# Optimization experiments

Measured on AMD Instinct MI355X. Metric: run time of the kernel, lower is better.

Reference implementation:

```python
import jax, jax.numpy as jnp
import numpy as np

D_MODEL = 1024
NUM_HEADS = 16
HEAD_DIM = D_MODEL // NUM_HEADS
FF_DIM = 4096
EPS = 1e-5


def _layer_norm(x, gamma, beta):
    mu = jnp.mean(x, axis=-1, keepdims=True)
    var = jnp.var(x, axis=-1, keepdims=True)
    return (x - mu) * jax.lax.rsqrt(var + EPS) * gamma + beta


def setup_inputs() -> dict:
    key0 = jax.random.key(0)
    ks = jax.random.split(key0, 20)
    s = 0.02
    B, S = 2, 2048
    inp = {
        'value': jax.random.normal(ks[0], (B, S, D_MODEL), jnp.float32),
        'key': jax.random.normal(ks[1], (B, S, D_MODEL), jnp.float32),
        'query': jax.random.normal(ks[2], (B, S, D_MODEL), jnp.float32),
        # attention projections (stored [in, out]; y = x @ W + b)
        'wq': jax.random.normal(ks[3], (D_MODEL, D_MODEL), jnp.float32) * s,
        'bq': jnp.zeros((D_MODEL,), jnp.float32),
        'wk': jax.random.normal(ks[4], (D_MODEL, D_MODEL), jnp.float32) * s,
        'bk': jnp.zeros((D_MODEL,), jnp.float32),
        'wv': jax.random.normal(ks[5], (D_MODEL, D_MODEL), jnp.float32) * s,
        'bv': jnp.zeros((D_MODEL,), jnp.float32),
        'wo': jax.random.normal(ks[6], (D_MODEL, D_MODEL), jnp.float32) * s,
        'bo': jnp.zeros((D_MODEL,), jnp.float32),
        # layernorm 1
        'g1': jnp.ones((D_MODEL,), jnp.float32),
        'beta1': jnp.zeros((D_MODEL,), jnp.float32),
        # feed-forward
        'w1': jax.random.normal(ks[7], (D_MODEL, FF_DIM), jnp.float32) * s,
        'b1': jnp.zeros((FF_DIM,), jnp.float32),
        'w2': jax.random.normal(ks[8], (FF_DIM, D_MODEL), jnp.float32) * s,
        'b2': jnp.zeros((D_MODEL,), jnp.float32),
        # layernorm 2
        'g2': jnp.ones((D_MODEL,), jnp.float32),
        'beta2': jnp.zeros((D_MODEL,), jnp.float32),
    }
    return inp


def reference(value, key, query, wq, bq, wk, bk, wv, bv, wo, bo,
              g1, beta1, w1, b1, w2, b2, g2, beta2):
    B, S, _ = query.shape
    # QKV projections -> [B, S, H, Dh]
    Q = (query @ wq + bq).reshape(B, S, NUM_HEADS, HEAD_DIM)
    K = (key @ wk + bk).reshape(B, S, NUM_HEADS, HEAD_DIM)
    V = (value @ wv + bv).reshape(B, S, NUM_HEADS, HEAD_DIM)
    # scaled dot-product attention (full score matrix, as in source)
    energy = jnp.einsum('bqhd,bkhd->bhqk', Q, K) / jnp.sqrt(jnp.float32(HEAD_DIM))
    attn = jax.nn.softmax(energy, axis=-1)
    out = jnp.einsum('bhqk,bkhd->bqhd', attn, V).reshape(B, S, D_MODEL)
    attn_out = out @ wo + bo
    # residual + norm1 (dropout is identity in eval)
    x = _layer_norm(attn_out + query, g1, beta1)
    # feed-forward
    ff = jax.nn.relu(x @ w1 + b1) @ w2 + b2
    # residual + norm2
    return _layer_norm(ff + x, g2, beta2)
```

## Files before the change

kernel.cpp:

```cpp
#include <hip/hip_runtime.h>
#include <hip/hip_bf16.h>
#include <cstdint>
#include <math.h>

typedef __bf16 bf16_t;
typedef __attribute__((ext_vector_type(2))) __bf16 bf16x2;
typedef __attribute__((ext_vector_type(4))) __bf16 bf16x4;
typedef __attribute__((ext_vector_type(8))) __bf16 bf16x8;
typedef __attribute__((ext_vector_type(4))) float f32x4;
typedef __attribute__((ext_vector_type(16))) float f32x16;
typedef __attribute__((ext_vector_type(2))) int int2v;
typedef __attribute__((ext_vector_type(4))) int int4v;

#define B_SZ 2
#define S_SZ 2048
#define D_MODEL 1024
#define NUM_HEADS 16
#define HEAD_DIM 64
#define FF_DIM 4096
#define M_ROWS (B_SZ * S_SZ)

#define CF 0.180336880f
#define THRC 2.0f

__device__ __forceinline__ float fexp2(float x) { return __builtin_amdgcn_exp2f(x); }

__device__ __forceinline__ void gload_lds16(const void* g, void* lds) {
    __builtin_amdgcn_global_load_lds(
        (const __attribute__((address_space(1))) void*)(uintptr_t)g,
        (__attribute__((address_space(3))) void*)(uint32_t)(uintptr_t)lds,
        16, 0, 0);
}

__device__ __forceinline__ f32x4 mfma16(bf16x8 a, bf16x8 b, f32x4 c) {
    return __builtin_amdgcn_mfma_f32_16x16x32_bf16(a, b, c, 0, 0, 0);
}
__device__ __forceinline__ f32x16 mfma32(bf16x8 a, bf16x8 b, f32x16 c) {
    return __builtin_amdgcn_mfma_f32_32x32x16_bf16(a, b, c, 0, 0, 0);
}
__device__ __forceinline__ int2v plswap(int a, int b) {
    return __builtin_amdgcn_permlane32_swap(a, b, false, false);
}
__device__ __forceinline__ int packbf(float a, float b) {
    bf16x2 t; t[0] = (bf16_t)a; t[1] = (bf16_t)b;
    return __builtin_bit_cast(int, t);
}

__device__ __forceinline__ int xcd_swz(int lin, int nwg) {
    return (lin & 7) * (nwg >> 3) + (lin >> 3);
}

__global__ __launch_bounds__(256) void cast3_f32_bf16(const float* __restrict__ in0,
                                                      const float* __restrict__ in1,
                                                      const float* __restrict__ in2,
                                                      bf16_t* __restrict__ out0,
                                                      bf16_t* __restrict__ out1,
                                                      bf16_t* __restrict__ out2) {
    int which = blockIdx.x >> 12;
    int blk = blockIdx.x & 4095;
    const float* in = which == 0 ? in0 : which == 1 ? in1 : in2;
    bf16_t* out = which == 0 ? out0 : which == 1 ? out1 : out2;
    size_t i = ((size_t)blk * 256 + threadIdx.x) * 4;
    float4 v = *(const float4*)(in + i);
    bf16x4 o;
    o[0] = (bf16_t)v.x; o[1] = (bf16_t)v.y; o[2] = (bf16_t)v.z; o[3] = (bf16_t)v.w;
    *(bf16x4*)(out + i) = o;
}

__global__ __launch_bounds__(256) void transpose_cast_w4(const float* __restrict__ W0,
                                                         const float* __restrict__ W1,
                                                         const float* __restrict__ W2,
                                                         const float* __restrict__ W3,
                                                         bf16_t* __restrict__ T0,
                                                         bf16_t* __restrict__ T1,
                                                         bf16_t* __restrict__ T2,
                                                         bf16_t* __restrict__ T3) {
    __shared__ float t[32][33];
    const int K = 1024, N = 1024;
    const float* W = blockIdx.z == 0 ? W0 : blockIdx.z == 1 ? W1 : blockIdx.z == 2 ? W2 : W3;
    bf16_t* WT = blockIdx.z == 0 ? T0 : blockIdx.z == 1 ? T1 : blockIdx.z == 2 ? T2 : T3;
    int tid = threadIdx.x;
    int rr = tid >> 3, cc = (tid & 7) * 4;
    int k0 = blockIdx.x * 32, n0 = blockIdx.y * 32;
    float4 v = *(const float4*)(W + (size_t)(k0 + rr) * N + n0 + cc);
    t[rr][cc + 0] = v.x; t[rr][cc + 1] = v.y; t[rr][cc + 2] = v.z; t[rr][cc + 3] = v.w;
    __syncthreads();
    bf16x4 o;
    o[0] = (bf16_t)t[cc + 0][rr]; o[1] = (bf16_t)t[cc + 1][rr];
    o[2] = (bf16_t)t[cc + 2][rr]; o[3] = (bf16_t)t[cc + 3][rr];
    *(bf16x4*)(WT + (size_t)(n0 + rr) * K + k0 + cc) = o;
}

__global__ __launch_bounds__(256) void transpose_cast_w(const float* __restrict__ W,
                                                        bf16_t* __restrict__ WT,
                                                        int K, int N) {
    __shared__ float t[32][33];
    int tid = threadIdx.x;
    int rr = tid >> 3, cc = (tid & 7) * 4;
    int k0 = blockIdx.x * 32, n0 = blockIdx.y * 32;
    float4 v = *(const float4*)(W + (size_t)(k0 + rr) * N + n0 + cc);
    t[rr][cc + 0] = v.x; t[rr][cc + 1] = v.y; t[rr][cc + 2] = v.z; t[rr][cc + 3] = v.w;
    __syncthreads();
    bf16x4 o;
    o[0] = (bf16_t)t[cc + 0][rr]; o[1] = (bf16_t)t[cc + 1][rr];
    o[2] = (bf16_t)t[cc + 2][rr]; o[3] = (bf16_t)t[cc + 3][rr];
    *(bf16x4*)(WT + (size_t)(n0 + rr) * K + k0 + cc) = o;
}

__global__ __launch_bounds__(256) void transpose_v(const bf16_t* __restrict__ Vp,
                                                   bf16_t* __restrict__ VT) {
    __shared__ bf16_t t[32][34];
    int tid = threadIdx.x;
    int rr = tid >> 3, cc = (tid & 7) * 4;
    int bh = blockIdx.z;
    int b = bh >> 4, h = bh & 15;
    int s0 = blockIdx.x * 32, d0 = blockIdx.y * 32;
    bf16x4 v = *(const bf16x4*)(Vp + ((size_t)(b * S_SZ + s0 + rr)) * D_MODEL + h * HEAD_DIM + d0 + cc);
    t[rr][cc + 0] = v[0]; t[rr][cc + 1] = v[1]; t[rr][cc + 2] = v[2]; t[rr][cc + 3] = v[3];
    __syncthreads();
    bf16x4 o;
    o[0] = t[cc + 0][rr]; o[1] = t[cc + 1][rr]; o[2] = t[cc + 2][rr]; o[3] = t[cc + 3][rr];
    *(bf16x4*)(VT + ((size_t)(bh * HEAD_DIM + d0 + rr)) * S_SZ + s0 + cc) = o;
}

template<int BNF, bool RELU, bool OUT_BF16, bool OUT_F32>
__device__ __forceinline__ void gemm_core256(const bf16_t* __restrict__ A, int lda,
                                             const bf16_t* __restrict__ Bt, int ldb,
                                             const float* __restrict__ bias, bool useBias,
                                             float* __restrict__ Cf,
                                             bf16_t* __restrict__ Cb,
                                             int N, int Klen, int m0, int n0,
                                             bf16_t* sA, bf16_t* sB) {
    const int tid = threadIdx.x;
    const int lane = tid & 63, w = tid >> 6;
    const int g = lane >> 4, r = lane & 15;
    const int wm = (w >> 2) * 128;
    const int wn = (w & 3) * (16 * BNF);
    const int ABUF = 8192;
    const int BBUF = (BNF == 4) ? 8192 : 4096;

    const bf16_t* Ablk = A + (size_t)m0 * lda;
    const bf16_t* Bblk = Bt + (size_t)n0 * ldb;
    const bf16_t* a0 = Ablk + (size_t)(tid >> 2) * lda + (tid & 3) * 8;
    const bf16_t* a1 = a0 + (size_t)128 * lda;
    const bf16_t* b0 = Bblk + (size_t)(tid >> 2) * ldb + (tid & 3) * 8;
    const bf16_t* b1 = b0 + (size_t)128 * ldb;

    f32x4 acc[8][BNF];
#pragma unroll
    for (int i = 0; i < 8; i++)
#pragma unroll
        for (int j = 0; j < BNF; j++)
#pragma unroll
            for (int e = 0; e < 4; e++) acc[i][j][e] = 0.f;

    auto stage = [&](int buf, int k0) {
        gload_lds16(a0 + k0, sA + buf * ABUF + tid * 8);
        gload_lds16(a1 + k0, sA + buf * ABUF + 4096 + tid * 8);
        gload_lds16(b0 + k0, sB + buf * BBUF + tid * 8);
        if (BNF == 4) gload_lds16(b1 + k0, sB + buf * BBUF + 4096 + tid * 8);
    };
    auto compute = [&](int buf) {
        bf16x8 a[8], b[BNF];
#pragma unroll
        for (int i = 0; i < 8; i++)
            a[i] = *(const bf16x8*)(sA + buf * ABUF + (wm + i * 16 + r) * 32 + g * 8);
#pragma unroll
        for (int j = 0; j < BNF; j++)
            b[j] = *(const bf16x8*)(sB + buf * BBUF + (wn + j * 16 + r) * 32 + g * 8);
#pragma unroll
        for (int i = 0; i < 8; i++)
#pragma unroll
            for (int j = 0; j < BNF; j++)
                acc[i][j] = mfma16(a[i], b[j], acc[i][j]);
    };

    const int nk = Klen >> 5;
    stage(0, 0);
    stage(1, 32);
    int bc = 0, bs = 2;
    for (int s = 0; s < nk; ++s) {
        if (s + 2 < nk) {
            stage(bs, (s + 2) * 32);
            if (BNF == 4) asm volatile("s_waitcnt vmcnt(8)" ::: "memory");
            else          asm volatile("s_waitcnt vmcnt(6)" ::: "memory");
        } else if (s + 1 < nk) {
            if (BNF == 4) asm volatile("s_waitcnt vmcnt(4)" ::: "memory");
            else          asm volatile("s_waitcnt vmcnt(3)" ::: "memory");
        } else {
            asm volatile("s_waitcnt vmcnt(0)" ::: "memory");
        }
        __builtin_amdgcn_s_barrier();
        __builtin_amdgcn_sched_barrier(0);
        compute(bc);
        __builtin_amdgcn_sched_barrier(0);
        __builtin_amdgcn_s_barrier();
        bc = (bc + 1 == 3) ? 0 : bc + 1;
        bs = (bs + 1 == 3) ? 0 : bs + 1;
    }

#pragma unroll
    for (int j = 0; j < BNF; j++) {
        int n = n0 + wn + j * 16 + r;
        float bv = useBias ? bias[n] : 0.f;
#pragma unroll
        for (int i = 0; i < 8; i++) {
#pragma unroll
            for (int rr = 0; rr < 4; rr++) {
                int mrow = m0 + wm + i * 16 + g * 4 + rr;
                float val = acc[i][j][rr] + bv;
                if (RELU) val = fmaxf(val, 0.f);
                if (OUT_F32) Cf[(size_t)mrow * N + n] = val;
                if (OUT_BF16) Cb[(size_t)mrow * N + n] = (bf16_t)val;
            }
        }
    }
}

template<int BNF, bool RELU, bool OUT_BF16, bool OUT_F32>
__global__ __launch_bounds__(512, 2) void gemm_bt256(const bf16_t* __restrict__ A, int lda,
                                                     const bf16_t* __restrict__ Bt, int ldb,
                                                     const float* __restrict__ bias,
                                                     float* __restrict__ Cf0,
                                                     float* __restrict__ Cf1,
                                                     bf16_t* __restrict__ Cb,
                                                     int N, int Klen) {
    __shared__ bf16_t sA[3 * 8192];
    __shared__ bf16_t sB[3 * ((BNF == 4) ? 8192 : 4096)];
    const int lin = blockIdx.x + gridDim.x * (blockIdx.y + gridDim.y * blockIdx.z);
    const int nwg = gridDim.x * gridDim.y * gridDim.z;
    const int swz = xcd_swz(lin, nwg);
    const int bx = swz % gridDim.x;
    const int rest = swz / gridDim.x;
    const int by = rest % gridDim.y;
    const int bz = rest / gridDim.y;
    const int koff = bz * Klen;
    gemm_core256<BNF, RELU, OUT_BF16, OUT_F32>(A + koff, lda, Bt + koff, ldb, bias, bz == 0,
                                               bz ? Cf1 : Cf0, Cb, N, Klen,
                                               bx * 256, by * (64 * BNF), sA, sB);
}

__global__ __launch_bounds__(512, 2) void gemm_qkv256(const bf16_t* __restrict__ A0,
                                                      const bf16_t* __restrict__ A1,
                                                      const bf16_t* __restrict__ A2,
                                                      const bf16_t* __restrict__ B0,
                                                      const bf16_t* __restrict__ B1,
                                                      const bf16_t* __restrict__ B2,
                                                      const float* __restrict__ b0,
                                                      const float* __restrict__ b1,
                                                      const float* __restrict__ b2,
                                                      bf16_t* __restrict__ C0,
                                                      bf16_t* __restrict__ C1,
                                                      bf16_t* __restrict__ C2) {
    __shared__ bf16_t sA[3 * 8192];
    __shared__ bf16_t sB[3 * 8192];
    const int lin = blockIdx.x + gridDim.x * (blockIdx.y + gridDim.y * blockIdx.z);
    const int nwg = gridDim.x * gridDim.y * gridDim.z;
    const int swz = xcd_swz(lin, nwg);
    const int bx = swz % gridDim.x;
    const int rest = swz / gridDim.x;
    const int by = rest % gridDim.y;
    const int bz = rest / gridDim.y;
    const bf16_t* A = bz == 0 ? A0 : bz == 1 ? A1 : A2;
    const bf16_t* Bt = bz == 0 ? B0 : bz == 1 ? B1 : B2;
    const float* bias = bz == 0 ? b0 : bz == 1 ? b1 : b2;
    bf16_t* C = bz == 0 ? C0 : bz == 1 ? C1 : C2;
    gemm_core256<4, false, true, false>(A, 1024, Bt, 1024, bias, true,
                                        nullptr, C, 1024, 1024, bx * 256, by * 256, sA, sB);
}

__device__ __forceinline__ void flash_tile(
    const char* kt, const char* vt, int l31, int hi,
    const bf16x8 (&bq)[4],
    f32x16& o0, f32x16& o1, float& mC, float& l_run)
{
    bf16x8 ak[4];
#pragma unroll
    for (int kb = 0; kb < 4; kb++)
        ak[kb] = *(const bf16x8*)(kt + l31 * 128 + (((kb << 1) | hi) ^ (l31 & 7)) * 16);
    bf16x8 av[4];
#pragma unroll
    for (int db = 0; db < 2; db++)
#pragma unroll
        for (int kb = 0; kb < 2; kb++)
            av[db * 2 + kb] = *(const bf16x8*)(vt + (db * 32 + l31) * 64 + ((((kb << 1) | hi)) ^ ((l31 >> 1) & 3)) * 16);

    f32x16 s;
#pragma unroll
    for (int e = 0; e < 16; e++) s[e] = 0.f;
#pragma unroll
    for (int kb = 0; kb < 4; kb++) s = mfma32(ak[kb], bq[kb], s);

    float ma = fmaxf(fmaxf(s[0], s[1]), fmaxf(s[2], s[3]));
    float mb = fmaxf(fmaxf(s[4], s[5]), fmaxf(s[6], s[7]));
    float mc = fmaxf(fmaxf(s[8], s[9]), fmaxf(s[10], s[11]));
    float md = fmaxf(fmaxf(s[12], s[13]), fmaxf(s[14], s[15]));
    float pmaxC = fmaxf(fmaxf(ma, mb), fmaxf(mc, md)) * CF;

    if (!__all(pmaxC <= mC + THRC)) {
        int2v pr = plswap(__float_as_int(pmaxC), __float_as_int(pmaxC));
        float rowmaxC = fmaxf(__int_as_float(pr[0]), __int_as_float(pr[1]));
        float mnewC = fmaxf(mC, rowmaxC);
        float alpha = fexp2(mC - mnewC);
        mC = mnewC;
        l_run *= alpha;
#pragma unroll
        for (int e = 0; e < 16; e++) { o0[e] *= alpha; o1[e] *= alpha; }
    }

#pragma unroll
    for (int e = 0; e < 16; e++) s[e] = fexp2(__builtin_fmaf(s[e], CF, -mC));
    float t0 = (s[0] + s[1]) + (s[2] + s[3]);
    float t1 = (s[4] + s[5]) + (s[6] + s[7]);
    float t2 = (s[8] + s[9]) + (s[10] + s[11]);
    float t3 = (s[12] + s[13]) + (s[14] + s[15]);
    l_run += (t0 + t1) + (t2 + t3);

#pragma unroll
    for (int kb2 = 0; kb2 < 2; kb2++) {
        const int bse = kb2 * 8;
        int W0 = packbf(s[bse + 0], s[bse + 1]);
        int W1 = packbf(s[bse + 2], s[bse + 3]);
        int W2 = packbf(s[bse + 4], s[bse + 5]);
        int W3 = packbf(s[bse + 6], s[bse + 7]);
        int2v r02 = plswap(W0, W2);
        int2v r13 = plswap(W1, W3);
        int4v fw; fw[0] = r02[0]; fw[1] = r13[0]; fw[2] = r02[1]; fw[3] = r13[1];
        bf16x8 pf = __builtin_bit_cast(bf16x8, fw);
        o0 = mfma32(av[kb2], pf, o0);
        o1 = mfma32(av[2 + kb2], pf, o1);
    }
}

__global__ __launch_bounds__(256) void flash_attn(const bf16_t* __restrict__ Qp,
                                                  const bf16_t* __restrict__ Kp,
                                                  const bf16_t* __restrict__ VT,
                                                  bf16_t* __restrict__ Oa) {
    __shared__ alignas(16) char lds[2][2][8192];
    const int tid = threadIdx.x;
    const int lane = tid & 63;
    const int wave = tid >> 6;
    const int half = wave >> 1;
    const int qt = wave & 1;
    const int l31 = lane & 31, hi = lane >> 5;

    const int lin = blockIdx.x + (blockIdx.y << 5) + (blockIdx.z << 9);
    const int swz = (lin & 7) * 128 + (lin >> 3);
    const int qb = swz & 31;
    const int h = (swz >> 5) & 15;
    const int b = swz >> 9;

    const int q0 = qb * 64 + qt * 32;

    const bf16_t* Qb = Qp + (size_t)b * S_SZ * D_MODEL + h * HEAD_DIM;
    const bf16_t* Kb = Kp + (size_t)b * S_SZ * D_MODEL + h * HEAD_DIM;
    const bf16_t* Vb = VT + ((size_t)(b * NUM_HEADS + h) * HEAD_DIM) * S_SZ;

    const int sh = wave & 1;
    const int skvbase = sh * (S_SZ / 2);
    const bool kRole = wave < 2;

    const bf16_t* src_run;
    size_t inner_stride;
    size_t tile_stride;
    char* dst0;
    char* dst1;
    if (kRole) {
        src_run = Kb + (size_t)(skvbase + (lane >> 3)) * D_MODEL + ((lane & 7) ^ (lane >> 3)) * 8;
        inner_stride = (size_t)8 * D_MODEL;
        tile_stride = (size_t)32 * D_MODEL;
        dst0 = &lds[0][sh][0] + lane * 16;
        dst1 = &lds[1][sh][0] + lane * 16;
    } else {
        src_run = Vb + (size_t)(lane >> 2) * S_SZ + skvbase + ((lane & 3) ^ ((lane >> 3) & 3)) * 8;
        inner_stride = (size_t)16 * S_SZ;
        tile_stride = 32;
        dst0 = &lds[0][sh][4096] + lane * 16;
        dst1 = &lds[1][sh][4096] + lane * 16;
    }

    bf16x8 bq[4];
#pragma unroll
    for (int kb = 0; kb < 4; kb++)
        bq[kb] = *(const bf16x8*)(Qb + (size_t)(q0 + l31) * D_MODEL + kb * 16 + hi * 8);

    f32x16 o0, o1;
#pragma unroll
    for (int e = 0; e < 16; e++) { o0[e] = 0.f; o1[e] = 0.f; }
    float mC = -1e30f, l_run = 0.f;

    const char* kt0 = &lds[0][half][0];
    const char* vt0 = &lds[0][half][4096];
    const char* kt1 = &lds[1][half][0];
    const char* vt1 = &lds[1][half][4096];

#pragma unroll
    for (int ii = 0; ii < 4; ii++)
        gload_lds16(src_run + ii * inner_stride, dst0 + ii * 1024);
    src_run += tile_stride;
    __syncthreads();

    for (int t = 0; t < 32; t += 2) {
#pragma unroll
        for (int ii = 0; ii < 4; ii++)
            gload_lds16(src_run + ii * inner_stride, dst1 + ii * 1024);
        src_run += tile_stride;
        flash_tile(kt0, vt0, l31, hi, bq, o0, o1, mC, l_run);
        __syncthreads();

        if (t + 2 < 32) {
#pragma unroll
            for (int ii = 0; ii < 4; ii++)
                gload_lds16(src_run + ii * inner_stride, dst0 + ii * 1024);
            src_run += tile_stride;
        }
        flash_tile(kt1, vt1, l31, hi, bq, o0, o1, mC, l_run);
        __syncthreads();
    }

    int2v lp = plswap(__float_as_int(l_run), __float_as_int(l_run));
    l_run = __int_as_float(lp[0]) + __int_as_float(lp[1]);

    float (*obuf)[2][64] = (float (*)[2][64])(&lds[0][0][0]);
    float (*mrg)[64][2] = (float (*)[64][2])(&lds[0][0][0] + 16384);
    if (half == 1) {
        mrg[qt][lane][0] = mC;
        mrg[qt][lane][1] = l_run;
#pragma unroll
        for (int e = 0; e < 16; e++) {
            obuf[e][qt][lane] = o0[e];
            obuf[16 + e][qt][lane] = o1[e];
        }
    }
    __syncthreads();
    if (half == 0) {
        const float m2C = mrg[qt][lane][0], l2 = mrg[qt][lane][1];
        const float mm = fmaxf(mC, m2C);
        const float e1 = fexp2(mC - mm);
        const float e2 = fexp2(m2C - mm);
        const float linv = 1.f / (l_run * e1 + l2 * e2);
        bf16_t* Orow = Oa + ((size_t)b * S_SZ + q0 + l31) * D_MODEL + h * HEAD_DIM;
#pragma unroll
        for (int db = 0; db < 2; db++) {
#pragma unroll
            for (int rq = 0; rq < 4; rq++) {
                bf16x4 st;
#pragma unroll
                for (int i = 0; i < 4; i++) {
                    const int e = rq * 4 + i;
                    const float own = db ? o1[e] : o0[e];
                    const float oth = obuf[db * 16 + e][qt][lane];
                    st[i] = (bf16_t)((own * e1 + oth * e2) * linv);
                }
                *(bf16x4*)(Orow + db * 32 + rq * 8 + hi * 4) = st;
            }
        }
    }
}

__global__ __launch_bounds__(256) void ln_fused(const float* __restrict__ A,
                                                const float* __restrict__ A2,
                                                const float* __restrict__ R,
                                                const float* __restrict__ gamma,
                                                const float* __restrict__ beta,
                                                float* __restrict__ Xf,
                                                bf16_t* __restrict__ Xb) {
    __shared__ float red[8];
    int row = blockIdx.x, tid = threadIdx.x;
    size_t base = (size_t)row * D_MODEL + tid * 4;
    float4 a = *(const float4*)(A + base);
    float4 rv = *(const float4*)(R + base);
    float v0 = a.x + rv.x, v1 = a.y + rv.y, v2 = a.z + rv.z, v3 = a.w + rv.w;
    if (A2) {
        float4 a2 = *(const float4*)(A2 + base);
        v0 += a2.x; v1 += a2.y; v2 += a2.z; v3 += a2.w;
    }
    float s = v0 + v1 + v2 + v3;
    float q = v0 * v0 + v1 * v1 + v2 * v2 + v3 * v3;
#pragma unroll
    for (int off = 32; off; off >>= 1) { s += __shfl_down(s, off); q += __shfl_down(q, off); }
    if ((tid & 63) == 0) { red[tid >> 6] = s; red[4 + (tid >> 6)] = q; }
    __syncthreads();
    s = red[0] + red[1] + red[2] + red[3];
    q = red[4] + red[5] + red[6] + red[7];
    float mean = s * (1.f / D_MODEL);
    float var = q * (1.f / D_MODEL) - mean * mean;
    float rstd = rsqrtf(var + 1e-5f);
    float4 gm = *(const float4*)(gamma + tid * 4);
    float4 bt = *(const float4*)(beta + tid * 4);
    float y0 = (v0 - mean) * rstd * gm.x + bt.x;
    float y1 = (v1 - mean) * rstd * gm.y + bt.y;
    float y2 = (v2 - mean) * rstd * gm.z + bt.z;
    float y3 = (v3 - mean) * rstd * gm.w + bt.w;
    float4 yo; yo.x = y0; yo.y = y1; yo.z = y2; yo.w = y3;
    *(float4*)(Xf + base) = yo;
    if (Xb) {
        bf16x4 ob; ob[0] = (bf16_t)y0; ob[1] = (bf16_t)y1; ob[2] = (bf16_t)y2; ob[3] = (bf16_t)y3;
        *(bf16x4*)(Xb + base) = ob;
    }
}

extern "C" void kernel_launch(void* const* d_in, const int* in_sizes, int n_in,
                              void* d_out, int out_size, void* d_ws, size_t ws_size,
                              hipStream_t stream) {
    const float* value = (const float*)d_in[0];
    const float* key   = (const float*)d_in[1];
    const float* query = (const float*)d_in[2];
    const float* wq = (const float*)d_in[3];
    const float* bq = (const float*)d_in[4];
    const float* wk = (const float*)d_in[5];
    const float* bk = (const float*)d_in[6];
    const float* wv = (const float*)d_in[7];
    const float* bv = (const float*)d_in[8];
    const float* wo = (const float*)d_in[9];
    const float* bo = (const float*)d_in[10];
    const float* g1 = (const float*)d_in[11];
    const float* beta1 = (const float*)d_in[12];
    const float* w1 = (const float*)d_in[13];
    const float* b1 = (const float*)d_in[14];
    const float* w2 = (const float*)d_in[15];
    const float* b2 = (const float*)d_in[16];
    const float* g2 = (const float*)d_in[17];
    const float* beta2 = (const float*)d_in[18];
    (void)in_sizes; (void)n_in; (void)out_size; (void)ws_size;

    const size_t MB = 1ull << 20;
    char* ws = (char*)d_ws;
    bf16_t* wqT = (bf16_t*)(ws + 0 * MB);
    bf16_t* wkT = (bf16_t*)(ws + 2 * MB);
    bf16_t* wvT = (bf16_t*)(ws + 4 * MB);
    bf16_t* woT = (bf16_t*)(ws + 6 * MB);
    bf16_t* w1T = (bf16_t*)(ws + 8 * MB);
    bf16_t* w2T = (bf16_t*)(ws + 16 * MB);
    bf16_t* q_bf = (bf16_t*)(ws + 24 * MB);
    bf16_t* k_bf = (bf16_t*)(ws + 32 * MB);
    bf16_t* v_bf = (bf16_t*)(ws + 40 * MB);
    bf16_t* Qp  = (bf16_t*)(ws + 48 * MB);
    bf16_t* Kp  = (bf16_t*)(ws + 56 * MB);
    bf16_t* Vp  = (bf16_t*)(ws + 64 * MB);
    bf16_t* VT  = (bf16_t*)(ws + 72 * MB);
    bf16_t* attn = (bf16_t*)(ws + 24 * MB);
    float*  woP0 = (float*)(ws + 32 * MB);
    float*  woP1 = (float*)(ws + 48 * MB);
    float*  x_f = (float*)(ws + 64 * MB);
    bf16_t* x_b = (bf16_t*)(ws + 24 * MB);
    bf16_t* h_b = (bf16_t*)(ws + 32 * MB);
    float*  ffP0 = (float*)(ws + 80 * MB);
    float*  ffP1 = (float*)(ws + 96 * MB);

    dim3 blk(256);
    dim3 blk512(512);

    cast3_f32_bf16<<<12288, blk, 0, stream>>>(query, key, value, q_bf, k_bf, v_bf);
    transpose_cast_w4<<<dim3(32, 32, 4), blk, 0, stream>>>(wq, wk, wv, wo, wqT, wkT, wvT, woT);
    transpose_cast_w<<<dim3(32, 128), blk, 0, stream>>>(w1, w1T, 1024, 4096);
    transpose_cast_w<<<dim3(128, 32), blk, 0, stream>>>(w2, w2T, 4096, 1024);

    gemm_qkv256<<<dim3(16, 4, 3), blk512, 0, stream>>>(q_bf, k_bf, v_bf, wqT, wkT, wvT,
                                                       bq, bk, bv, Qp, Kp, Vp);

    transpose_v<<<dim3(64, 2, 32), blk, 0, stream>>>(Vp, VT);

    flash_attn<<<dim3(32, 16, 2), blk, 0, stream>>>(Qp, Kp, VT, attn);

    gemm_bt256<2, false, false, true><<<dim3(16, 8, 2), blk512, 0, stream>>>(attn, 1024, woT, 1024, bo, woP0, woP1, nullptr, D_MODEL, 512);

    ln_fused<<<4096, blk, 0, stream>>>(woP0, woP1, query, g1, beta1, x_f, x_b);

    gemm_bt256<4, true, true, false><<<dim3(16, 16, 1), blk512, 0, stream>>>(x_b, 1024, w1T, 1024, b1, nullptr, nullptr, h_b, FF_DIM, 1024);

    gemm_bt256<2, false, false, true><<<dim3(16, 8, 2), blk512, 0, stream>>>(h_b, 4096, w2T, 4096, b2, ffP0, ffP1, nullptr, D_MODEL, 2048);

    ln_fused<<<4096, blk, 0, stream>>>(ffP0, ffP1, x_f, g2, beta2, (float*)d_out, nullptr);
}
```

Measured before the change: 259.7 us.

## Rewrite GEMM core with 64-wide K tiles, swizzled LDS, interleaved quad-phase pipeline

Replaces the triple-buffered 32-wide-K GEMM mainloop with a double-buffered 64-wide-K loop. Each tile is split into four read/compute phases, and the global-to-LDS loads for the next tile are spread between them. Shared-memory rows are XOR-swizzled to avoid bank conflicts, and MFMA sections raise wave priority with s_setprio. Launch bounds drop to one 512-thread block per CU because LDS use is larger, which trades occupancy for deeper per-block overlap and adds many more barriers per tile.

```diff
diff --git a/kernel.cpp b/kernel.cpp
--- a/kernel.cpp
+++ b/kernel.cpp
@@ -124,27 +124,25 @@
 }
 
 template<int BNF, bool RELU, bool OUT_BF16, bool OUT_F32>
-__device__ __forceinline__ void gemm_core256(const bf16_t* __restrict__ A, int lda,
-                                             const bf16_t* __restrict__ Bt, int ldb,
-                                             const float* __restrict__ bias, bool useBias,
-                                             float* __restrict__ Cf,
-                                             bf16_t* __restrict__ Cb,
-                                             int N, int Klen, int m0, int n0,
-                                             bf16_t* sA, bf16_t* sB) {
+__device__ __forceinline__ void gemm8p_core(const bf16_t* __restrict__ Ag, int lda,
+                                            const bf16_t* __restrict__ Bg, int ldb,
+                                            const float* __restrict__ bias, bool useBias,
+                                            float* __restrict__ Cf,
+                                            bf16_t* __restrict__ Cb,
+                                            int N, int Klen, int m0, int n0,
+                                            bf16_t* sA, bf16_t* sB) {
+    constexpr int BSTRIDE = (BNF == 4) ? 16384 : 8192;
     const int tid = threadIdx.x;
     const int lane = tid & 63, w = tid >> 6;
     const int g = lane >> 4, r = lane & 15;
-    const int wm = (w >> 2) * 128;
-    const int wn = (w & 3) * (16 * BNF);
-    const int ABUF = 8192;
-    const int BBUF = (BNF == 4) ? 8192 : 4096;
-
-    const bf16_t* Ablk = A + (size_t)m0 * lda;
-    const bf16_t* Bblk = Bt + (size_t)n0 * ldb;
-    const bf16_t* a0 = Ablk + (size_t)(tid >> 2) * lda + (tid & 3) * 8;
-    const bf16_t* a1 = a0 + (size_t)128 * lda;
-    const bf16_t* b0 = Bblk + (size_t)(tid >> 2) * ldb + (tid & 3) * 8;
-    const bf16_t* b1 = b0 + (size_t)128 * ldb;
+    const int ah = w >> 2;
+    const int bh = (BNF == 4) ? ((w & 3) >> 1) : 0;
+    const int wbr = (BNF == 4) ? ((w & 1) * 64) : ((w & 3) * 32);
+    const int rs = r & 7;
+
+    const int scol = ((tid & 7) ^ ((tid >> 3) & 7)) * 8;
+    const bf16_t* aSrc = Ag + (size_t)(m0 + (tid >> 3)) * lda + scol;
+    const bf16_t* bSrc = Bg + (size_t)(n0 + (tid >> 3)) * ldb + scol;
 
     f32x4 acc[8][BNF];
 #pragma unroll
@@ -154,60 +152,101 @@
 #pragma unroll
             for (int e = 0; e < 4; e++) acc[i][j][e] = 0.f;
 
-    auto stage = [&](int buf, int k0) {
-        gload_lds16(a0 + k0, sA + buf * ABUF + tid * 8);
-        gload_lds16(a1 + k0, sA + buf * ABUF + 4096 + tid * 8);
-        gload_lds16(b0 + k0, sB + buf * BBUF + tid * 8);
-        if (BNF == 4) gload_lds16(b1 + k0, sB + buf * BBUF + 4096 + tid * 8);
+    auto stageA = [&](int buf, int half, int k0) {
+        const bf16_t* s = aSrc + (size_t)(half * 128) * lda + k0;
+        bf16_t* d = sA + buf * 16384 + half * 8192 + tid * 8;
+        gload_lds16(s, d);
+        gload_lds16(s + (size_t)64 * lda, d + 4096);
     };
-    auto compute = [&](int buf) {
-        bf16x8 a[8], b[BNF];
-#pragma unroll
-        for (int i = 0; i < 8; i++)
-            a[i] = *(const bf16x8*)(sA + buf * ABUF + (wm + i * 16 + r) * 32 + g * 8);
-#pragma unroll
-        for (int j = 0; j < BNF; j++)
-            b[j] = *(const bf16x8*)(sB + buf * BBUF + (wn + j * 16 + r) * 32 + g * 8);
-#pragma unroll
-        for (int i = 0; i < 8; i++)
-#pragma unroll
-            for (int j = 0; j < BNF; j++)
-                acc[i][j] = mfma16(a[i], b[j], acc[i][j]);
+    auto stageB = [&](int buf, int half, int k0) {
+        const bf16_t* s = bSrc + (size_t)(half * 128) * ldb + k0;
+        bf16_t* d = sB + buf * BSTRIDE + half * 8192 + tid * 8;
+        gload_lds16(s, d);
+        gload_lds16(s + (size_t)64 * ldb, d + 4096);
     };
 
-    const int nk = Klen >> 5;
-    stage(0, 0);
-    stage(1, 32);
-    int bc = 0, bs = 2;
-    for (int s = 0; s < nk; ++s) {
-        if (s + 2 < nk) {
-            stage(bs, (s + 2) * 32);
-            if (BNF == 4) asm volatile("s_waitcnt vmcnt(8)" ::: "memory");
-            else          asm volatile("s_waitcnt vmcnt(6)" ::: "memory");
-        } else if (s + 1 < nk) {
-            if (BNF == 4) asm volatile("s_waitcnt vmcnt(4)" ::: "memory");
-            else          asm volatile("s_waitcnt vmcnt(3)" ::: "memory");
-        } else {
-            asm volatile("s_waitcnt vmcnt(0)" ::: "memory");
+    bf16x8 af[4][2];
+    bf16x8 bfr[BNF / 2][2];
+
+    auto READ = [&](int buf, int ih, int jsel) {
+        const bf16_t* mA = sA + buf * 16384 + ah * 8192;
+        const bf16_t* mB = sB + buf * BSTRIDE + bh * 8192;
+#pragma unroll
+        for (int ii = 0; ii < 4; ii++) {
+            const int rho = ih + ii * 16 + r;
+#pragma unroll
+            for (int kk = 0; kk < 2; kk++)
+                af[ii][kk] = *(const bf16x8*)(mA + rho * 64 + (((kk << 2) | g) ^ rs) * 8);
         }
-        __builtin_amdgcn_s_barrier();
-        __builtin_amdgcn_sched_barrier(0);
-        compute(bc);
-        __builtin_amdgcn_sched_barrier(0);
-        __builtin_amdgcn_s_barrier();
-        bc = (bc + 1 == 3) ? 0 : bc + 1;
-        bs = (bs + 1 == 3) ? 0 : bs + 1;
-    }
+#pragma unroll
+        for (int jj = 0; jj < BNF / 2; jj++) {
+            const int rho = wbr + jsel * (BNF == 4 ? 32 : 16) + jj * 16 + r;
+#pragma unroll
+            for (int kk = 0; kk < 2; kk++)
+                bfr[jj][kk] = *(const bf16x8*)(mB + rho * 64 + (((kk << 2) | g) ^ rs) * 8);
+        }
+    };
+    auto QUAD = [&](int ih4, int jsel) {
+        __builtin_amdgcn_s_setprio(1);
+#pragma unroll
+        for (int ii = 0; ii < 4; ii++)
+#pragma unroll
+            for (int jj = 0; jj < BNF / 2; jj++)
+#pragma unroll
+                for (int kk = 0; kk < 2; kk++)
+                    acc[ih4 + ii][jsel * (BNF / 2) + jj] =
+                        mfma16(af[ii][kk], bfr[jj][kk], acc[ih4 + ii][jsel * (BNF / 2) + jj]);
+        __builtin_amdgcn_s_setprio(0);
+    };
+
+#define LGKM0() do { asm volatile("s_waitcnt lgkmcnt(0)" ::: "memory"); \
+                     __builtin_amdgcn_sched_barrier(0); } while (0)
+
+    const int nk = Klen >> 6;
+    stageA(0, 0, 0); stageA(0, 1, 0); stageB(0, 0, 0);
+    if constexpr (BNF == 4) stageB(0, 1, 0);
+
+    for (int t = 0; t < nk; ++t) {
+        const int buf = t & 1, nb = buf ^ 1;
+        const int kn = (t + 1) << 6;
+        const bool hn = (t + 1 < nk);
+        if (hn) { stageA(nb, 0, kn); asm volatile("s_waitcnt vmcnt(2)" ::: "memory"); }
+        else    { asm volatile("s_waitcnt vmcnt(0)" ::: "memory"); }
+        __builtin_amdgcn_s_barrier();
+        READ(buf, 0, 0);
+        LGKM0();
+        QUAD(0, 0);
+        __builtin_amdgcn_s_barrier();
+        READ(buf, 0, 1);
+        if (hn) stageA(nb, 1, kn);
+        __builtin_amdgcn_s_barrier();
+        LGKM0();
+        QUAD(0, 1);
+        __builtin_amdgcn_s_barrier();
+        READ(buf, 64, 0);
+        if (hn) stageB(nb, 0, kn);
+        __builtin_amdgcn_s_barrier();
+        LGKM0();
+        QUAD(4, 0);
+        __builtin_amdgcn_s_barrier();
+        READ(buf, 64, 1);
+        if constexpr (BNF == 4) { if (hn) stageB(nb, 1, kn); }
+        __builtin_amdgcn_s_barrier();
+        LGKM0();
+        QUAD(4, 1);
+        __builtin_amdgcn_s_barrier();
+    }
+#undef LGKM0
 
 #pragma unroll
     for (int j = 0; j < BNF; j++) {
-        int n = n0 + wn + j * 16 + r;
+        int n = n0 + (w & 3) * (16 * BNF) + j * 16 + r;
         float bv = useBias ? bias[n] : 0.f;
 #pragma unroll
         for (int i = 0; i < 8; i++) {
 #pragma unroll
             for (int rr = 0; rr < 4; rr++) {
-                int mrow = m0 + wm + i * 16 + g * 4 + rr;
+                int mrow = m0 + (w >> 2) * 128 + i * 16 + g * 4 + rr;
                 float val = acc[i][j][rr] + bv;
                 if (RELU) val = fmaxf(val, 0.f);
                 if (OUT_F32) Cf[(size_t)mrow * N + n] = val;
@@ -218,55 +257,56 @@
 }
 
 template<int BNF, bool RELU, bool OUT_BF16, bool OUT_F32>
-__global__ __launch_bounds__(512, 2) void gemm_bt256(const bf16_t* __restrict__ A, int lda,
-                                                     const bf16_t* __restrict__ Bt, int ldb,
-                                                     const float* __restrict__ bias,
-                                                     float* __restrict__ Cf0,
-                                                     float* __restrict__ Cf1,
-                                                     bf16_t* __restrict__ Cb,
-                                                     int N, int Klen) {
-    __shared__ bf16_t sA[3 * 8192];
-    __shared__ bf16_t sB[3 * ((BNF == 4) ? 8192 : 4096)];
+__global__ __launch_bounds__(512, 1) void gemm8p(const bf16_t* __restrict__ A, int lda,
+                                                 const bf16_t* __restrict__ Bt, int ldb,
+                                                 const float* __restrict__ bias,
+                                                 float* __restrict__ Cf0,
+                                                 float* __restrict__ Cf1,
+                                                 bf16_t* __restrict__ Cb,
+                                                 int N, int Klen) {
+    __shared__ bf16_t sA[2 * 16384];
+    __shared__ bf16_t sB[2 * ((BNF == 4) ? 16384 : 8192)];
     const int lin = blockIdx.x + gridDim.x * (blockIdx.y + gridDim.y * blockIdx.z);
     const int nwg = gridDim.x * gridDim.y * gridDim.z;
-    const int swz = xcd_swz(lin, nwg);
-    const int bx = swz % gridDim.x;
-    const int rest = swz / gridDim.x;
+    const int sz = xcd_swz(lin, nwg);
+    const int bx = sz % gridDim.x;
+    const int rest = sz / gridDim.x;
     const int by = rest % gridDim.y;
     const int bz = rest / gridDim.y;
     const int koff = bz * Klen;
-    gemm_core256<BNF, RELU, OUT_BF16, OUT_F32>(A + koff, lda, Bt + koff, ldb, bias, bz == 0,
-                                               bz ? Cf1 : Cf0, Cb, N, Klen,
-                                               bx * 256, by * (64 * BNF), sA, sB);
-}
-
-__global__ __launch_bounds__(512, 2) void gemm_qkv256(const bf16_t* __restrict__ A0,
-                                                      const bf16_t* __restrict__ A1,
-                                                      const bf16_t* __restrict__ A2,
-                                                      const bf16_t* __restrict__ B0,
-                                                      const bf16_t* __restrict__ B1,
-                                                      const bf16_t* __restrict__ B2,
-                                                      const float* __restrict__ b0,
-                                                      const float* __restrict__ b1,
-                                                      const float* __restrict__ b2,
-                                                      bf16_t* __restrict__ C0,
-                                                      bf16_t* __restrict__ C1,
-                                                      bf16_t* __restrict__ C2) {
-    __shared__ bf16_t sA[3 * 8192];
-    __shared__ bf16_t sB[3 * 8192];
+    gemm8p_core<BNF, RELU, OUT_BF16, OUT_F32>(A + koff, lda, Bt + koff, ldb,
+                                              bias, bz == 0,
+                                              bz ? Cf1 : Cf0, Cb, N, Klen,
+                                              bx * 256, by * (64 * BNF), sA, sB);
+}
+
+__global__ __launch_bounds__(512, 1) void gemm_qkv8p(const bf16_t* __restrict__ A0,
+                                                     const bf16_t* __restrict__ A1,
+                                                     const bf16_t* __restrict__ A2,
+                                                     const bf16_t* __restrict__ B0,
+                                                     const bf16_t* __restrict__ B1,
+                                                     const bf16_t* __restrict__ B2,
+                                                     const float* __restrict__ b0,
+                                                     const float* __restrict__ b1,
+                                                     const float* __restrict__ b2,
+                                                     bf16_t* __restrict__ C0,
+                                                     bf16_t* __restrict__ C1,
+                                                     bf16_t* __restrict__ C2) {
+    __shared__ bf16_t sA[2 * 16384];
+    __shared__ bf16_t sB[2 * 16384];
     const int lin = blockIdx.x + gridDim.x * (blockIdx.y + gridDim.y * blockIdx.z);
     const int nwg = gridDim.x * gridDim.y * gridDim.z;
-    const int swz = xcd_swz(lin, nwg);
-    const int bx = swz % gridDim.x;
-    const int rest = swz / gridDim.x;
+    const int sz = xcd_swz(lin, nwg);
+    const int bx = sz % gridDim.x;
+    const int rest = sz / gridDim.x;
     const int by = rest % gridDim.y;
     const int bz = rest / gridDim.y;
     const bf16_t* A = bz == 0 ? A0 : bz == 1 ? A1 : A2;
     const bf16_t* Bt = bz == 0 ? B0 : bz == 1 ? B1 : B2;
     const float* bias = bz == 0 ? b0 : bz == 1 ? b1 : b2;
     bf16_t* C = bz == 0 ? C0 : bz == 1 ? C1 : C2;
-    gemm_core256<4, false, true, false>(A, 1024, Bt, 1024, bias, true,
-                                        nullptr, C, 1024, 1024, bx * 256, by * 256, sA, sB);
+    gemm8p_core<4, false, true, false>(A, 1024, Bt, 1024, bias, true,
+                                       nullptr, C, 1024, 1024, bx * 256, by * 256, sA, sB);
 }
 
 __device__ __forceinline__ void flash_tile(
@@ -556,20 +596,20 @@
     transpose_cast_w<<<dim3(32, 128), blk, 0, stream>>>(w1, w1T, 1024, 4096);
     transpose_cast_w<<<dim3(128, 32), blk, 0, stream>>>(w2, w2T, 4096, 1024);
 
-    gemm_qkv256<<<dim3(16, 4, 3), blk512, 0, stream>>>(q_bf, k_bf, v_bf, wqT, wkT, wvT,
-                                                       bq, bk, bv, Qp, Kp, Vp);
+    gemm_qkv8p<<<dim3(16, 4, 3), blk512, 0, stream>>>(q_bf, k_bf, v_bf, wqT, wkT, wvT,
+                                                      bq, bk, bv, Qp, Kp, Vp);
 
     transpose_v<<<dim3(64, 2, 32), blk, 0, stream>>>(Vp, VT);
 
     flash_attn<<<dim3(32, 16, 2), blk, 0, stream>>>(Qp, Kp, VT, attn);
 
-    gemm_bt256<2, false, false, true><<<dim3(16, 8, 2), blk512, 0, stream>>>(attn, 1024, woT, 1024, bo, woP0, woP1, nullptr, D_MODEL, 512);
+    gemm8p<2, false, false, true><<<dim3(16, 8, 2), blk512, 0, stream>>>(attn, 1024, woT, 1024, bo, woP0, woP1, nullptr, D_MODEL, 512);
 
     ln_fused<<<4096, blk, 0, stream>>>(woP0, woP1, query, g1, beta1, x_f, x_b);
 
-    gemm_bt256<4, true, true, false><<<dim3(16, 16, 1), blk512, 0, stream>>>(x_b, 1024, w1T, 1024, b1, nullptr, nullptr, h_b, FF_DIM, 1024);
-
-    gemm_bt256<2, false, false, true><<<dim3(16, 8, 2), blk512, 0, stream>>>(h_b, 4096, w2T, 4096, b2, ffP0, ffP1, nullptr, D_MODEL, 2048);
+    gemm8p<4, true, true, false><<<dim3(16, 16, 1), blk512, 0, stream>>>(x_b, 1024, w1T, 1024, b1, nullptr, nullptr, h_b, FF_DIM, 1024);
+
+    gemm8p<2, false, false, true><<<dim3(16, 8, 2), blk512, 0, stream>>>(h_b, 4096, w2T, 4096, b2, ffP0, ffP1, nullptr, D_MODEL, 2048);
 
     ln_fused<<<4096, blk, 0, stream>>>(ffP0, ffP1, x_f, g2, beta2, (float*)d_out, nullptr);
 }
```

New measurement: 266.2 us. +2.5%, slower.
